# Kernel tuning notes

Measured on AMD Instinct MI355X. Metric: run time of the kernel, lower is better.

Reference implementation:

```python
import jax, jax.numpy as jnp
import numpy as np

N, E, D_IN, H = 4096, 1024, 256, 64
THETA = 0.01
LN_EPS = 1e-5


def _layer_norm(x, w, b):
    m = x.mean(-1, keepdims=True)
    v = ((x - m) ** 2).mean(-1, keepdims=True)
    return (x - m) * jax.lax.rsqrt(v + LN_EPS) * w + b


def setup_inputs() -> dict:
    key = jax.random.key(0)
    ks = jax.random.split(key, 8)
    xav = lambda k, shp: jax.random.normal(k, shp, jnp.float32) * np.float32(np.sqrt(2.0 / (shp[0] + shp[1])))
    return {
        "adj": jax.random.uniform(ks[0], (N, E), jnp.float32),
        "G": jax.random.normal(ks[1], (N, N), jnp.float32) * 0.02,
        "feats": jax.random.normal(ks[2], (N, D_IN), jnp.float32),
        "W_v_w": xav(ks[3], (H, D_IN)),
        "lin_w": xav(ks[4], (H, D_IN)),
        "w_o_w": xav(ks[5], (1, H)),
        "w_o_b": jnp.zeros((1,), jnp.float32),
        "ln1_w": jnp.ones((H,), jnp.float32),
        "ln1_b": jnp.zeros((H,), jnp.float32),
        "ln2_w": jnp.ones((H,), jnp.float32),
        "ln2_b": jnp.zeros((H,), jnp.float32),
        "kn": 10,
    }


def reference(adj, G, feats, W_v_w, lin_w, w_o_w, w_o_b, ln1_w, ln1_b, ln2_w, ln2_b, kn):
    # adj: (N, E) incidence; torch code transposes then uses adj.t() again,
    # so e_center = feats.T @ adj / edge_degree  -> (D_IN, E)
    e_center = (feats.T @ adj) / adj.sum(0)[None, :]
    f = feats @ W_v_w.T                                   # (N, H) values
    scores = (f @ f.T) / np.float32(np.sqrt(H))           # (N, N)
    attn = jax.nn.softmax(scores, axis=1)
    s = _layer_norm(e_center.T @ lin_w.T, ln1_w, ln1_b)   # (E, H)
    d = _layer_norm(attn @ f, ln2_w, ln2_b)               # (N, H)
    # hadamard_power: scores[m,n] = sum_k w[k]*(s[m,k]-d[n,k])^2 + b
    # expanded to avoid the (E*N, H) broadcast the torch code materializes
    w = w_o_w[0]                                          # (H,)
    ta = ((s * s) @ w)[:, None] + ((d * d) @ w)[None, :] - 2.0 * ((s * w) @ d.T) + w_o_b[0]
    ta = jnp.exp(-ta / np.float32(2 * 20 ** 2))           # (E, N)
    Hm = ta.T                                             # (N, E) soft incidence
    # Generate_G_from_H with unit edge weights, done via row/col scaling
    DV = Hm.sum(1)
    DE = Hm.sum(0)
    invDE = jnp.where(DE > 0, 1.0 / DE, 0.0)
    invDV = jnp.where(DV > 0, DV ** -0.5, 0.0)
    A = (invDV[:, None] * Hm) * invDE[None, :]            # DV2 @ H @ W @ invDE
    B = Hm * invDV[:, None]                               # (DV2 @ H).T side
    G_new = A @ B.T                                       # (N, N)
    return (1.0 - THETA) * G + THETA * G_new
```

## Files before the change

kernel.cpp:

```cpp
#include <hip/hip_runtime.h>
#include <hip/hip_bf16.h>
#include <math.h>

#define NN 4096
#define NE 1024
#define DIN 256
#define HD 64

typedef __hip_bfloat16 bf16;
__device__ __forceinline__ float b2f(bf16 x){ return __bfloat162float(x); }

typedef __attribute__((ext_vector_type(8))) short s16x8;
typedef __attribute__((ext_vector_type(4))) float f32x4;

__device__ __forceinline__ unsigned short f2b_rne(float x){
  unsigned u; __builtin_memcpy(&u, &x, 4);
  u += 0x7fff + ((u>>16)&1);
  return (unsigned short)(u>>16);
}

#define STAGE128(dstbase, PA, strideA, PB, strideB, k0) do{ \
  _Pragma("unroll") \
  for (int it_ = 0; it_ < 4; ++it_){ \
    int r_  = it_*32 + (t>>3); \
    int ss_ = ((t&7) ^ (r_&7))*8; \
    __builtin_amdgcn_global_load_lds( \
      (const __attribute__((address_space(1))) void*)((PA) + (size_t)r_*(strideA) + (k0) + ss_), \
      (__attribute__((address_space(3))) void*)((dstbase) + it_*4096 + t*16), 16, 0, 0); \
    __builtin_amdgcn_global_load_lds( \
      (const __attribute__((address_space(1))) void*)((PB) + (size_t)r_*(strideB) + (k0) + ss_), \
      (__attribute__((address_space(3))) void*)((dstbase) + 16384 + it_*4096 + t*16), 16, 0, 0); \
  } }while(0)

#define COMPUTE64(base) do{ \
  _Pragma("unroll") \
  for (int kk_ = 0; kk_ < 2; ++kk_){ \
    s16x8 a_[4], b_[4]; \
    _Pragma("unroll") \
    for (int mi_ = 0; mi_ < 4; ++mi_){ \
      int row_ = wr*64 + mi_*16 + (lane & 15); \
      int s_   = kk_*4 + (lane >> 4); \
      a_[mi_] = *(const s16x8*)((base) + row_*128 + ((s_ ^ (row_&7))*16)); \
    } \
    _Pragma("unroll") \
    for (int ni_ = 0; ni_ < 4; ++ni_){ \
      int row_ = wc*64 + ni_*16 + (lane & 15); \
      int s_   = kk_*4 + (lane >> 4); \
      b_[ni_] = *(const s16x8*)((base) + 16384 + row_*128 + ((s_ ^ (row_&7))*16)); \
    } \
    _Pragma("unroll") \
    for (int mi_ = 0; mi_ < 4; ++mi_) \
      _Pragma("unroll") \
      for (int ni_ = 0; ni_ < 4; ++ni_) \
        acc[mi_][ni_] = __builtin_amdgcn_mfma_f32_16x16x32_bf16(a_[mi_], b_[ni_], acc[mi_][ni_], 0, 0, 0); \
  } }while(0)

__global__ void k_t2b(const float* __restrict__ src, unsigned short* __restrict__ dst,
                      float* __restrict__ csum){
  __shared__ float Ls[64][65];
  int R = gridDim.x*64, C = gridDim.y*64;
  int r0 = blockIdx.x*64, c0 = blockIdx.y*64;
  int t = threadIdx.x;
  int lr = t>>2, lc = (t&3)*16;
  #pragma unroll
  for (int s = 0; s < 4; ++s){
    float4 v = *(const float4*)(src + (size_t)(r0+lr)*C + c0 + lc + s*4);
    Ls[lr][lc+s*4+0]=v.x; Ls[lr][lc+s*4+1]=v.y; Ls[lr][lc+s*4+2]=v.z; Ls[lr][lc+s*4+3]=v.w;
  }
  __syncthreads();
  if (csum != nullptr && t < 64){
    float s = 0.f;
    #pragma unroll
    for (int r = 0; r < 64; ++r) s += Ls[r][t];
    atomicAdd(&csum[c0 + t], s);
  }
  int wc = t>>3, wr8 = (t&7)*8;
  #pragma unroll
  for (int p = 0; p < 2; ++p){
    int c = wc + p*32;
    s16x8 o;
    #pragma unroll
    for (int e = 0; e < 8; ++e) o[e] = (short)f2b_rne(Ls[wr8+e][c]);
    *(s16x8*)(dst + (size_t)(c0+c)*R + r0 + wr8) = o;
  }
}

__global__ void __launch_bounds__(256, 2)
k_ect_mfma(const unsigned short* __restrict__ fT, const unsigned short* __restrict__ aT,
           float* __restrict__ ecT){
  __shared__ __align__(16) unsigned char sm[65536];
  const int t = threadIdx.x, lane = t & 63, w = t >> 6;
  const int wr = w >> 1, wc = w & 1;
  const int m0 = blockIdx.x*128, n0 = blockIdx.y*128, kb = blockIdx.z*256;
  const unsigned short* PA = fT + (size_t)m0*NN + kb;
  const unsigned short* PB = aT + (size_t)n0*NN + kb;
  f32x4 acc[4][4] = {};
  STAGE128(sm, PA, NN, PB, NN, 0);
  __syncthreads();
  int cur = 0;
  for (int kt = 0; kt < 4; ++kt){
    if (kt < 3) STAGE128(sm + (cur^1)*32768, PA, NN, PB, NN, (kt+1)*64);
    COMPUTE64(sm + cur*32768);
    __syncthreads();
    cur ^= 1;
  }
  #pragma unroll
  for (int mi = 0; mi < 4; ++mi)
    #pragma unroll
    for (int q = 0; q < 4; ++q){
      int c = m0 + wr*64 + mi*16 + (lane>>4)*4 + q;
      #pragma unroll
      for (int ni = 0; ni < 4; ++ni){
        int e = n0 + wc*64 + ni*16 + (lane & 15);
        atomicAdd(&ecT[(size_t)e*DIN + c], acc[mi][ni][q]);
      }
    }
}

__global__ void k_s(const float* __restrict__ ecT, const float* __restrict__ colsum,
                    const float* __restrict__ lin_w,
                    const float* __restrict__ ln1w, const float* __restrict__ ln1b,
                    const float* __restrict__ wow,
                    float* __restrict__ sw, float* __restrict__ sq_s){
  int e = blockIdx.x, h = threadIdx.x;
  const float* row = ecT + (size_t)e*DIN;
  const float* lw  = lin_w + (size_t)h*DIN;
  float acc = 0.f;
  for (int c = 0; c < DIN; ++c) acc += row[c]*lw[c];
  acc /= colsum[e];
  float tot = acc;
  for (int m=32;m>=1;m>>=1) tot += __shfl_xor(tot,m);
  float mean = tot*(1.f/64.f);
  float dv = acc - mean;
  float vv = dv*dv;
  for (int m=32;m>=1;m>>=1) vv += __shfl_xor(vv,m);
  float y = dv*(1.f/sqrtf(vv*(1.f/64.f)+1e-5f))*ln1w[h] + ln1b[h];
  float wv = wow[h];
  sw[(size_t)e*HD + h] = y*wv;
  float q = wv*y*y;
  for (int m=32;m>=1;m>>=1) q += __shfl_xor(q,m);
  if (h==0) sq_s[e] = q;
}

__global__ void k_f(const float* __restrict__ feats, const float* __restrict__ Wv,
                    float* __restrict__ f){
  __shared__ float As[64][65];
  __shared__ float Bs[64][65];
  int i0 = blockIdx.x*64;
  int c0 = blockIdx.y*64;
  int tid=threadIdx.x, tx=tid&15, ty=tid>>4;
  float acc[4][4]={};
  for (int idx=tid; idx<4096; idx+=256){
    int r=idx>>6, c=idx&63;
    As[c][r] = feats[(size_t)(i0+r)*DIN + c0+c];
    Bs[c][r] = Wv   [(size_t)r*DIN      + c0+c];
  }
  __syncthreads();
  for (int k=0;k<64;++k){
    float a[4], b[4];
    #pragma unroll
    for (int i=0;i<4;++i) a[i] = As[k][tx*4+i];
    #pragma unroll
    for (int i=0;i<4;++i) b[i] = Bs[k][ty*4+i];
    #pragma unroll
    for (int mi=0;mi<4;++mi)
      #pragma unroll
      for (int ni=0;ni<4;++ni) acc[mi][ni] += a[mi]*b[ni];
  }
  for (int mi=0;mi<4;++mi)
    for (int ni=0;ni<4;++ni)
      atomicAdd(&f[(size_t)(i0+tx*4+mi)*HD + ty*4+ni], acc[mi][ni]);
}

__global__ void k_f2b(const float* __restrict__ f, unsigned short* __restrict__ fb,
                      unsigned short* __restrict__ fbT){
  __shared__ unsigned short Ls[64][72];
  int n0 = blockIdx.x*64;
  int t = threadIdx.x;
  int r = t>>2, c0 = (t&3)*16;
  unsigned short tmp[16];
  #pragma unroll
  for (int s=0;s<16;++s) tmp[s] = f2b_rne(f[(size_t)(n0+r)*HD + c0 + s]);
  s16x8 v0, v1;
  #pragma unroll
  for (int e=0;e<8;++e){ v0[e] = (short)tmp[e]; v1[e] = (short)tmp[8+e]; }
  *(s16x8*)(fb + (size_t)(n0+r)*HD + c0)     = v0;
  *(s16x8*)(fb + (size_t)(n0+r)*HD + c0 + 8) = v1;
  #pragma unroll
  for (int s=0;s<16;++s) Ls[c0+s][r] = tmp[s];
  __syncthreads();
  int h = t>>2, n1 = (t&3)*16;
  s16x8 w0, w1;
  #pragma unroll
  for (int e=0;e<8;++e){ w0[e] = (short)Ls[h][n1+e]; w1[e] = (short)Ls[h][n1+8+e]; }
  *(s16x8*)(fbT + (size_t)h*NN + n0 + n1)     = w0;
  *(s16x8*)(fbT + (size_t)h*NN + n0 + n1 + 8) = w1;
}

__global__ void __launch_bounds__(256)
k_attn(const unsigned short* __restrict__ fb, const unsigned short* __restrict__ fbT,
       float* __restrict__ dpre, float* __restrict__ rowsum){
  __shared__ __align__(16) unsigned char sm[32768];
  const int t  = threadIdx.x;
  const int l  = t & 63;
  const int w  = t >> 6;
  const int g  = l >> 4;
  const int i0 = blockIdx.x*64;
  const int jb0 = blockIdx.y*256;

  s16x8 aQ[2];
  {
    const unsigned short* src = fb + (size_t)(i0 + w*16 + (l&15))*HD + g*8;
    aQ[0] = *(const s16x8*)(src);
    aQ[1] = *(const s16x8*)(src + 32);
  }

  f32x4 acco[4];
  #pragma unroll
  for (int nh=0;nh<4;++nh)
    #pragma unroll
    for (int q=0;q<4;++q) acco[nh][q] = 0.f;
  float rsum[4] = {0.f,0.f,0.f,0.f};

  float* Pw = (float*)(sm + 16384 + w*4096);

  for (int jt = 0; jt < 4; ++jt){
    int j0 = jb0 + jt*64;
    __syncthreads();
    #pragma unroll
    for (int p = 0; p < 2; ++p){
      int r  = p*32 + (t>>3);
      int cs = ((t&7) ^ (r&7))*8;
      __builtin_amdgcn_global_load_lds(
        (const __attribute__((address_space(1))) void*)(fb + (size_t)(j0+r)*HD + cs),
        (__attribute__((address_space(3))) void*)(sm + p*4096 + t*16), 16, 0, 0);
      __builtin_amdgcn_global_load_lds(
        (const __attribute__((address_space(1))) void*)(fbT + (size_t)r*NN + j0 + cs),
        (__attribute__((address_space(3))) void*)(sm + 8192 + p*4096 + t*16), 16, 0, 0);
    }
    __syncthreads();

    f32x4 accs[4];
    #pragma unroll
    for (int nj=0;nj<4;++nj)
      #pragma unroll
      for (int q=0;q<4;++q) accs[nj][q] = 0.f;
    #pragma unroll
    for (int kk=0; kk<2; ++kk){
      int s = kk*4 + g;
      #pragma unroll
      for (int nj=0;nj<4;++nj){
        int row = nj*16 + (l&15);
        s16x8 b = *(const s16x8*)(sm + row*128 + ((s ^ (row&7))*16));
        accs[nj] = __builtin_amdgcn_mfma_f32_16x16x32_bf16(aQ[kk], b, accs[nj], 0,0,0);
      }
    }

    #pragma unroll
    for (int q=0;q<4;++q){
      int i  = g*4 + q;
      int sw = (i&7)<<2;
      #pragma unroll
      for (int nj=0;nj<4;++nj){
        float p = __expf(accs[nj][q]*0.125f);
        rsum[q] += p;
        Pw[i*64 + ((nj*16 + (l&15)) ^ sw)] = p;
      }
    }

    #pragma unroll
    for (int kk=0; kk<2; ++kk){
      int i  = l & 15;
      int sw = (i&7)<<2;
      int jb = g*8 + kk*32;
      f32x4 va = *(const f32x4*)(Pw + i*64 + ( jb      ^ sw));
      f32x4 vb = *(const f32x4*)(Pw + i*64 + ((jb + 4) ^ sw));
      s16x8 pa;
      #pragma unroll
      for (int e=0;e<4;++e){
        float fa = va[e], fbv = vb[e];
        pa[e]   = (short)f2b_rne(fa);
        pa[4+e] = (short)f2b_rne(fbv);
      }
      int s = kk*4 + g;
      #pragma unroll
      for (int nh=0;nh<4;++nh){
        int row = nh*16 + (l&15);
        s16x8 bT = *(const s16x8*)(sm + 8192 + row*128 + ((s ^ (row&7))*16));
        acco[nh] = __builtin_amdgcn_mfma_f32_16x16x32_bf16(pa, bT, acco[nh], 0,0,0);
      }
    }
  }

  #pragma unroll
  for (int q=0;q<4;++q){
    float v = rsum[q];
    v += __shfl_xor(v,1); v += __shfl_xor(v,2);
    v += __shfl_xor(v,4); v += __shfl_xor(v,8);
    if ((l&15)==0) atomicAdd(&rowsum[i0 + w*16 + g*4 + q], v);
  }
  #pragma unroll
  for (int nh=0;nh<4;++nh)
    #pragma unroll
    for (int q=0;q<4;++q)
      atomicAdd(&dpre[(size_t)(i0 + w*16 + g*4 + q)*HD + nh*16 + (l&15)], acco[nh][q]);
}

__global__ void k_dln(const float* __restrict__ dpre, const float* __restrict__ rowsum,
                      const float* __restrict__ ln2w, const float* __restrict__ ln2b,
                      const float* __restrict__ wow,
                      float* __restrict__ dmat, float* __restrict__ sq_d){
  int lane = threadIdx.x & 63;
  int n = blockIdx.x*4 + (threadIdx.x>>6);
  float x = dpre[(size_t)n*HD + lane] / rowsum[n];
  float tot = x;
  for (int m=32;m>=1;m>>=1) tot += __shfl_xor(tot,m);
  float mean = tot*(1.f/64.f);
  float dv = x - mean;
  float vv = dv*dv;
  for (int m=32;m>=1;m>>=1) vv += __shfl_xor(vv,m);
  float y = dv*(1.f/sqrtf(vv*(1.f/64.f)+1e-5f))*ln2w[lane] + ln2b[lane];
  dmat[(size_t)n*HD + lane] = y;
  float wv = wow[lane];
  float q = wv*y*y;
  for (int m=32;m>=1;m>>=1) q += __shfl_xor(q,m);
  if (lane==0) sq_d[n] = q;
}

__global__ void k_hm(const float* __restrict__ dmat, const float* __restrict__ sw,
                     const float* __restrict__ sq_d, const float* __restrict__ sq_s,
                     const float* __restrict__ wob, bf16* __restrict__ Hm){
  __shared__ float As[64][65];
  __shared__ float Bs[64][65];
  int n0 = blockIdx.x*64, e0 = blockIdx.y*64;
  int tid=threadIdx.x, tx=tid&15, ty=tid>>4;
  for (int idx=tid; idx<4096; idx+=256){
    int r=idx>>6, c=idx&63;
    As[c][r] = dmat[(size_t)(n0+r)*HD + c];
    Bs[c][r] = sw  [(size_t)(e0+r)*HD + c];
  }
  __syncthreads();
  float acc[4][4]={};
  for (int k=0;k<64;++k){
    float a[4], b[4];
    #pragma unroll
    for (int i=0;i<4;++i) a[i] = As[k][tx*4+i];
    #pragma unroll
    for (int i=0;i<4;++i) b[i] = Bs[k][ty*4+i];
    #pragma unroll
    for (int mi=0;mi<4;++mi)
      #pragma unroll
      for (int ni=0;ni<4;++ni) acc[mi][ni] += a[mi]*b[ni];
  }
  float bias = wob[0];
  for (int mi=0;mi<4;++mi)
    for (int ni=0;ni<4;++ni){
      int nn = n0+tx*4+mi, ee = e0+ty*4+ni;
      float ta = sq_s[ee] + sq_d[nn] - 2.f*acc[mi][ni] + bias;
      float arg = -ta*(1.f/800.f);
      if (!(arg > -88.f)) arg = -88.f;
      if (arg > 60.f)     arg = 60.f;
      Hm[(size_t)nn*NE + ee] = __float2bfloat16(__expf(arg));
    }
}

__global__ void k_dv(const bf16* __restrict__ Hm, float* __restrict__ invDV){
  __shared__ float sm[256];
  int n = blockIdx.x, t = threadIdx.x;
  const bf16* row = Hm + (size_t)n*NE;
  float a = b2f(row[t]) + b2f(row[t+256]) + b2f(row[t+512]) + b2f(row[t+768]);
  sm[t]=a; __syncthreads();
  for (int s=128;s>0;s>>=1){ if(t<s) sm[t]+=sm[t+s]; __syncthreads(); }
  if (t==0){ float v = sm[0]; invDV[n] = (v>0.f) ? 1.f/sqrtf(v) : 0.f; }
}

__global__ void k_de(const bf16* __restrict__ Hm, float* __restrict__ DE){
  int e  = blockIdx.x*256 + threadIdx.x;
  int i0 = blockIdx.y*128;
  float acc=0.f;
  for (int i=0;i<128;++i) acc += b2f(Hm[(size_t)(i0+i)*NE + e]);
  atomicAdd(&DE[e], acc);
}
__global__ void k_invde(float* __restrict__ DE){
  int e = blockIdx.x*256 + threadIdx.x;
  float v = DE[e];
  DE[e] = (v>0.f) ? rsqrtf(v) : 0.f;
}

__global__ void k_scale(bf16* __restrict__ Hm, const float* __restrict__ rde){
  int idx = blockIdx.x*256 + threadIdx.x;
  int row = idx >> 7, c8 = idx & 127;
  size_t base = (size_t)row*NE + c8*8;
  s16x8 v = *(const s16x8*)(Hm + base);
  s16x8 o;
  #pragma unroll
  for (int j = 0; j < 8; ++j){
    unsigned int ww = ((unsigned int)(unsigned short)v[j]) << 16;
    float fv; __builtin_memcpy(&fv, &ww, 4);
    fv *= rde[c8*8 + j];
    o[j] = (short)f2b_rne(fv);
  }
  *(s16x8*)(Hm + base) = o;
}

__global__ void __launch_bounds__(256, 2)
k_final(const bf16* __restrict__ A2, const float* __restrict__ invDV,
        const float* __restrict__ G, float* __restrict__ out){
  __shared__ __align__(16) unsigned char sm[65536];
  const int t    = threadIdx.x;
  const int lane = t & 63;
  const int w    = t >> 6;
  const int wr   = w >> 1, wc = w & 1;

  int idx = blockIdx.x;
  int bi = (int)(32.5f - sqrtf(32.5f*32.5f - 2.f*(float)idx));
  while ((bi+1)*32 - ((bi+1)*bi)/2 <= idx) ++bi;
  while (bi*32 - (bi*(bi-1))/2 > idx) --bi;
  int bj = bi + (idx - (bi*32 - (bi*(bi-1))/2));
  const int i0 = bi*128, j0 = bj*128;

  const bf16* PA = A2 + (size_t)i0*NE;
  const bf16* PB = A2 + (size_t)j0*NE;

  f32x4 acc[4][4] = {};
  STAGE128(sm, PA, NE, PB, NE, 0);
  __syncthreads();
  int cur = 0;
  for (int kt = 0; kt < 16; ++kt){
    if (kt < 15) STAGE128(sm + (cur^1)*32768, PA, NE, PB, NE, (kt+1)*64);
    COMPUTE64(sm + cur*32768);
    __syncthreads();
    cur ^= 1;
  }

  float dvi[4][4], dvj[4];
  #pragma unroll
  for (int mi = 0; mi < 4; ++mi)
    #pragma unroll
    for (int q = 0; q < 4; ++q)
      dvi[mi][q] = invDV[i0 + wr*64 + mi*16 + (lane>>4)*4 + q];
  #pragma unroll
  for (int ni = 0; ni < 4; ++ni)
    dvj[ni] = invDV[j0 + wc*64 + ni*16 + (lane & 15)];

  #pragma unroll
  for (int mi = 0; mi < 4; ++mi)
    #pragma unroll
    for (int q = 0; q < 4; ++q){
      int ii = i0 + wr*64 + mi*16 + (lane>>4)*4 + q;
      #pragma unroll
      for (int ni = 0; ni < 4; ++ni){
        int jj = j0 + wc*64 + ni*16 + (lane & 15);
        size_t o = (size_t)ii*NN + jj;
        out[o] = 0.99f*G[o] + 0.01f*(dvi[mi][q]*dvj[ni]*acc[mi][ni][q]);
      }
    }

  if (bi == bj) return;
  float (*Mir)[64][65] = (float(*)[64][65])sm;
  for (int p = 0; p < 2; ++p){
    if (wr == p){
      #pragma unroll
      for (int mi = 0; mi < 4; ++mi)
        #pragma unroll
        for (int ni = 0; ni < 4; ++ni)
          #pragma unroll
          for (int q = 0; q < 4; ++q)
            Mir[wc][ni*16 + (lane & 15)][mi*16 + (lane>>4)*4 + q] =
              0.01f*(dvi[mi][q]*dvj[ni]*acc[mi][ni][q]);
    }
    __syncthreads();
    #pragma unroll
    for (int b = 0; b < 2; ++b){
      for (int itr = 0; itr < 16; ++itr){
        int idx2 = itr*256 + t;
        int jl = idx2 >> 6, il = idx2 & 63;
        size_t o = (size_t)(j0 + b*64 + jl)*NN + (i0 + p*64 + il);
        out[o] = 0.99f*G[o] + Mir[b][jl][il];
      }
    }
    __syncthreads();
  }
}

extern "C" void kernel_launch(void* const* d_in, const int* in_sizes, int n_in,
                              void* d_out, int out_size, void* d_ws, size_t ws_size,
                              hipStream_t stream){
  const float* adj  = (const float*)d_in[0];
  const float* G    = (const float*)d_in[1];
  const float* feats= (const float*)d_in[2];
  const float* Wv   = (const float*)d_in[3];
  const float* lin  = (const float*)d_in[4];
  const float* wow  = (const float*)d_in[5];
  const float* wob  = (const float*)d_in[6];
  const float* ln1w = (const float*)d_in[7];
  const float* ln1b = (const float*)d_in[8];
  const float* ln2w = (const float*)d_in[9];
  const float* ln2b = (const float*)d_in[10];
  float* out = (float*)d_out;

  float* w = (float*)d_ws;
  float* colsum = w; w += NE;
  float* DE     = w; w += NE;
  float* sq_s   = w; w += NE;
  float* rowsum = w; w += NN;
  float* sq_d   = w; w += NN;
  float* invDV  = w; w += NN;
  float* ecT    = w; w += NE*DIN;
  float* swp    = w; w += NE*HD;
  float* f      = w; w += NN*HD;
  float* dpre   = w; w += NN*HD;
  float* dmat   = w; w += NN*HD;
  unsigned short* fbm    = (unsigned short*)w; w += NN*HD/2;
  unsigned short* fbT    = (unsigned short*)w; w += NN*HD/2;
  unsigned short* featsT = (unsigned short*)w; w += NN*DIN/2;
  bf16*  Hm     = (bf16*)w;
  unsigned short* adjT = (unsigned short*)Hm;

  hipMemsetAsync(colsum, 0, NE*sizeof(float), stream);
  hipMemsetAsync(DE,     0, NE*sizeof(float), stream);
  hipMemsetAsync(rowsum, 0, NN*sizeof(float), stream);
  hipMemsetAsync(ecT,    0, (size_t)NE*DIN*sizeof(float), stream);
  hipMemsetAsync(f,      0, (size_t)NN*HD*sizeof(float), stream);
  hipMemsetAsync(dpre,   0, (size_t)NN*HD*sizeof(float), stream);

  k_t2b     <<<dim3(64,4),   256, 0, stream>>>(feats, featsT, nullptr);
  k_t2b     <<<dim3(64,16),  256, 0, stream>>>(adj, adjT, colsum);
  k_ect_mfma<<<dim3(2,8,16), 256, 0, stream>>>(featsT, adjT, ecT);
  k_s       <<<NE,            64, 0, stream>>>(ecT, colsum, lin, ln1w, ln1b, wow, swp, sq_s);
  k_f       <<<dim3(64,4),   256, 0, stream>>>(feats, Wv, f);
  k_f2b     <<<64,           256, 0, stream>>>(f, fbm, fbT);
  k_attn    <<<dim3(64,16),  256, 0, stream>>>(fbm, fbT, dpre, rowsum);
  k_dln     <<<NN/4,         256, 0, stream>>>(dpre, rowsum, ln2w, ln2b, wow, dmat, sq_d);
  k_hm      <<<dim3(64,16),  256, 0, stream>>>(dmat, swp, sq_d, sq_s, wob, Hm);
  k_dv      <<<NN,           256, 0, stream>>>(Hm, invDV);
  k_de      <<<dim3(4,32),   256, 0, stream>>>(Hm, DE);
  k_invde   <<<4,            256, 0, stream>>>(DE);
  k_scale   <<<2048,         256, 0, stream>>>(Hm, DE);
  k_final   <<<528,          256, 0, stream>>>(Hm, invDV, G, out);
}
```

Baseline: 354.2 us.

## Use bf16 MFMA for Hm distance GEMM and coalesce final output epilogue

The s·w and d matrices are now stored as bf16, and the Hm kernel computes the cross term with 16x16x32 bf16 MFMA instructions. The B tile is loaded into swizzled LDS through global_load_lds, replacing the fp32 scalar-FMA shared-memory GEMM. Separately, k_final stages the whole 128x128 result tile in LDS and writes both the direct and mirrored output blocks with float4-coalesced reads of G and writes of out. Previously the direct writes were strided scalars and the mirror used two scalar passes. The bf16 cross term adds rounding error to the exponent argument of Hm, and the larger LDS tile may affect occupancy of k_final.

After: 341.6 us. 1.04x faster.

```diff
diff --git a/kernel.cpp b/kernel.cpp
--- a/kernel.cpp
+++ b/kernel.cpp
@@ -121,7 +121,7 @@
                     const float* __restrict__ lin_w,
                     const float* __restrict__ ln1w, const float* __restrict__ ln1b,
                     const float* __restrict__ wow,
-                    float* __restrict__ sw, float* __restrict__ sq_s){
+                    unsigned short* __restrict__ swb, float* __restrict__ sq_s){
   int e = blockIdx.x, h = threadIdx.x;
   const float* row = ecT + (size_t)e*DIN;
   const float* lw  = lin_w + (size_t)h*DIN;
@@ -136,7 +136,7 @@
   for (int m=32;m>=1;m>>=1) vv += __shfl_xor(vv,m);
   float y = dv*(1.f/sqrtf(vv*(1.f/64.f)+1e-5f))*ln1w[h] + ln1b[h];
   float wv = wow[h];
-  sw[(size_t)e*HD + h] = y*wv;
+  swb[(size_t)e*HD + h] = f2b_rne(y*wv);
   float q = wv*y*y;
   for (int m=32;m>=1;m>>=1) q += __shfl_xor(q,m);
   if (h==0) sq_s[e] = q;
@@ -309,7 +309,7 @@
 __global__ void k_dln(const float* __restrict__ dpre, const float* __restrict__ rowsum,
                       const float* __restrict__ ln2w, const float* __restrict__ ln2b,
                       const float* __restrict__ wow,
-                      float* __restrict__ dmat, float* __restrict__ sq_d){
+                      unsigned short* __restrict__ dmatb, float* __restrict__ sq_d){
   int lane = threadIdx.x & 63;
   int n = blockIdx.x*4 + (threadIdx.x>>6);
   float x = dpre[(size_t)n*HD + lane] / rowsum[n];
@@ -320,48 +320,68 @@
   float vv = dv*dv;
   for (int m=32;m>=1;m>>=1) vv += __shfl_xor(vv,m);
   float y = dv*(1.f/sqrtf(vv*(1.f/64.f)+1e-5f))*ln2w[lane] + ln2b[lane];
-  dmat[(size_t)n*HD + lane] = y;
+  dmatb[(size_t)n*HD + lane] = f2b_rne(y);
   float wv = wow[lane];
   float q = wv*y*y;
   for (int m=32;m>=1;m>>=1) q += __shfl_xor(q,m);
   if (lane==0) sq_d[n] = q;
 }
 
-__global__ void k_hm(const float* __restrict__ dmat, const float* __restrict__ sw,
-                     const float* __restrict__ sq_d, const float* __restrict__ sq_s,
-                     const float* __restrict__ wob, bf16* __restrict__ Hm){
-  __shared__ float As[64][65];
-  __shared__ float Bs[64][65];
-  int n0 = blockIdx.x*64, e0 = blockIdx.y*64;
-  int tid=threadIdx.x, tx=tid&15, ty=tid>>4;
-  for (int idx=tid; idx<4096; idx+=256){
-    int r=idx>>6, c=idx&63;
-    As[c][r] = dmat[(size_t)(n0+r)*HD + c];
-    Bs[c][r] = sw  [(size_t)(e0+r)*HD + c];
-  }
-  __syncthreads();
-  float acc[4][4]={};
-  for (int k=0;k<64;++k){
-    float a[4], b[4];
-    #pragma unroll
-    for (int i=0;i<4;++i) a[i] = As[k][tx*4+i];
-    #pragma unroll
-    for (int i=0;i<4;++i) b[i] = Bs[k][ty*4+i];
-    #pragma unroll
-    for (int mi=0;mi<4;++mi)
-      #pragma unroll
-      for (int ni=0;ni<4;++ni) acc[mi][ni] += a[mi]*b[ni];
+__global__ void __launch_bounds__(256)
+k_hm(const unsigned short* __restrict__ dmatb, const unsigned short* __restrict__ swb,
+     const float* __restrict__ sq_d, const float* __restrict__ sq_s,
+     const float* __restrict__ wob, bf16* __restrict__ Hm){
+  __shared__ __align__(16) unsigned char sm[8192];
+  const int t = threadIdx.x, l = t & 63, w = t >> 6, g = l >> 4;
+  const int n0 = blockIdx.x*64, e0 = blockIdx.y*64;
+  #pragma unroll
+  for (int p = 0; p < 2; ++p){
+    int r  = p*32 + (t>>3);
+    int cs = ((t&7) ^ (r&7))*8;
+    __builtin_amdgcn_global_load_lds(
+      (const __attribute__((address_space(1))) void*)(swb + (size_t)(e0+r)*HD + cs),
+      (__attribute__((address_space(3))) void*)(sm + p*4096 + t*16), 16, 0, 0);
+  }
+  s16x8 aQ[2];
+  {
+    const unsigned short* src = dmatb + (size_t)(n0 + w*16 + (l&15))*HD + g*8;
+    aQ[0] = *(const s16x8*)(src);
+    aQ[1] = *(const s16x8*)(src + 32);
+  }
+  f32x4 accs[4];
+  #pragma unroll
+  for (int nj=0;nj<4;++nj)
+    #pragma unroll
+    for (int q=0;q<4;++q) accs[nj][q] = 0.f;
+  __syncthreads();
+  #pragma unroll
+  for (int kk=0; kk<2; ++kk){
+    int s = kk*4 + g;
+    #pragma unroll
+    for (int nj=0;nj<4;++nj){
+      int row = nj*16 + (l&15);
+      s16x8 b = *(const s16x8*)(sm + row*128 + ((s ^ (row&7))*16));
+      accs[nj] = __builtin_amdgcn_mfma_f32_16x16x32_bf16(aQ[kk], b, accs[nj], 0,0,0);
+    }
   }
   float bias = wob[0];
-  for (int mi=0;mi<4;++mi)
-    for (int ni=0;ni<4;++ni){
-      int nn = n0+tx*4+mi, ee = e0+ty*4+ni;
-      float ta = sq_s[ee] + sq_d[nn] - 2.f*acc[mi][ni] + bias;
+  float sqd[4];
+  #pragma unroll
+  for (int q=0;q<4;++q) sqd[q] = sq_d[n0 + w*16 + g*4 + q];
+  #pragma unroll
+  for (int nj=0;nj<4;++nj){
+    int e = e0 + nj*16 + (l&15);
+    float sqs = sq_s[e];
+    #pragma unroll
+    for (int q=0;q<4;++q){
+      float ta = sqs + sqd[q] - 2.f*accs[nj][q] + bias;
       float arg = -ta*(1.f/800.f);
       if (!(arg > -88.f)) arg = -88.f;
       if (arg > 60.f)     arg = 60.f;
-      Hm[(size_t)nn*NE + ee] = __float2bfloat16(__expf(arg));
-    }
+      int n = n0 + w*16 + g*4 + q;
+      Hm[(size_t)n*NE + e] = __float2bfloat16(__expf(arg));
+    }
+  }
 }
 
 __global__ void k_dv(const bf16* __restrict__ Hm, float* __restrict__ invDV){
@@ -406,7 +426,7 @@
 __global__ void __launch_bounds__(256, 2)
 k_final(const bf16* __restrict__ A2, const float* __restrict__ invDV,
         const float* __restrict__ G, float* __restrict__ out){
-  __shared__ __align__(16) unsigned char sm[65536];
+  __shared__ __align__(16) unsigned char sm[128*132*4];
   const int t    = threadIdx.x;
   const int lane = t & 63;
   const int w    = t >> 6;
@@ -443,43 +463,46 @@
   for (int ni = 0; ni < 4; ++ni)
     dvj[ni] = invDV[j0 + wc*64 + ni*16 + (lane & 15)];
 
+  float (*T)[132] = (float(*)[132])sm;
   #pragma unroll
   for (int mi = 0; mi < 4; ++mi)
     #pragma unroll
-    for (int q = 0; q < 4; ++q){
-      int ii = i0 + wr*64 + mi*16 + (lane>>4)*4 + q;
-      #pragma unroll
-      for (int ni = 0; ni < 4; ++ni){
-        int jj = j0 + wc*64 + ni*16 + (lane & 15);
-        size_t o = (size_t)ii*NN + jj;
-        out[o] = 0.99f*G[o] + 0.01f*(dvi[mi][q]*dvj[ni]*acc[mi][ni][q]);
-      }
-    }
+    for (int ni = 0; ni < 4; ++ni)
+      #pragma unroll
+      for (int q = 0; q < 4; ++q)
+        T[wr*64 + mi*16 + (lane>>4)*4 + q][wc*64 + ni*16 + (lane & 15)] =
+          0.01f*(dvi[mi][q]*dvj[ni]*acc[mi][ni][q]);
+  __syncthreads();
+
+  #pragma unroll
+  for (int it = 0; it < 16; ++it){
+    int idx2 = it*256 + t;
+    int il = idx2 >> 5;
+    int jc = (idx2 & 31)*4;
+    size_t o = (size_t)(i0+il)*NN + j0 + jc;
+    float4 gv = *(const float4*)(G + o);
+    float4 r;
+    r.x = 0.99f*gv.x + T[il][jc+0];
+    r.y = 0.99f*gv.y + T[il][jc+1];
+    r.z = 0.99f*gv.z + T[il][jc+2];
+    r.w = 0.99f*gv.w + T[il][jc+3];
+    *(float4*)(out + o) = r;
+  }
 
   if (bi == bj) return;
-  float (*Mir)[64][65] = (float(*)[64][65])sm;
-  for (int p = 0; p < 2; ++p){
-    if (wr == p){
-      #pragma unroll
-      for (int mi = 0; mi < 4; ++mi)
-        #pragma unroll
-        for (int ni = 0; ni < 4; ++ni)
-          #pragma unroll
-          for (int q = 0; q < 4; ++q)
-            Mir[wc][ni*16 + (lane & 15)][mi*16 + (lane>>4)*4 + q] =
-              0.01f*(dvi[mi][q]*dvj[ni]*acc[mi][ni][q]);
-    }
-    __syncthreads();
-    #pragma unroll
-    for (int b = 0; b < 2; ++b){
-      for (int itr = 0; itr < 16; ++itr){
-        int idx2 = itr*256 + t;
-        int jl = idx2 >> 6, il = idx2 & 63;
-        size_t o = (size_t)(j0 + b*64 + jl)*NN + (i0 + p*64 + il);
-        out[o] = 0.99f*G[o] + Mir[b][jl][il];
-      }
-    }
-    __syncthreads();
+  #pragma unroll
+  for (int it = 0; it < 16; ++it){
+    int idx2 = it*256 + t;
+    int jl = idx2 >> 5;
+    int ic = (idx2 & 31)*4;
+    size_t o = (size_t)(j0+jl)*NN + i0 + ic;
+    float4 gv = *(const float4*)(G + o);
+    float4 r;
+    r.x = 0.99f*gv.x + T[ic+0][jl];
+    r.y = 0.99f*gv.y + T[ic+1][jl];
+    r.z = 0.99f*gv.z + T[ic+2][jl];
+    r.w = 0.99f*gv.w + T[ic+3][jl];
+    *(float4*)(out + o) = r;
   }
 }
 
@@ -507,10 +530,10 @@
   float* sq_d   = w; w += NN;
   float* invDV  = w; w += NN;
   float* ecT    = w; w += NE*DIN;
-  float* swp    = w; w += NE*HD;
   float* f      = w; w += NN*HD;
   float* dpre   = w; w += NN*HD;
-  float* dmat   = w; w += NN*HD;
+  unsigned short* swb    = (unsigned short*)w; w += NE*HD/2;
+  unsigned short* dmatb  = (unsigned short*)w; w += NN*HD/2;
   unsigned short* fbm    = (unsigned short*)w; w += NN*HD/2;
   unsigned short* fbT    = (unsigned short*)w; w += NN*HD/2;
   unsigned short* featsT = (unsigned short*)w; w += NN*DIN/2;
@@ -527,12 +550,12 @@
   k_t2b     <<<dim3(64,4),   256, 0, stream>>>(feats, featsT, nullptr);
   k_t2b     <<<dim3(64,16),  256, 0, stream>>>(adj, adjT, colsum);
   k_ect_mfma<<<dim3(2,8,16), 256, 0, stream>>>(featsT, adjT, ecT);
-  k_s       <<<NE,            64, 0, stream>>>(ecT, colsum, lin, ln1w, ln1b, wow, swp, sq_s);
+  k_s       <<<NE,            64, 0, stream>>>(ecT, colsum, lin, ln1w, ln1b, wow, swb, sq_s);
   k_f       <<<dim3(64,4),   256, 0, stream>>>(feats, Wv, f);
   k_f2b     <<<64,           256, 0, stream>>>(f, fbm, fbT);
   k_attn    <<<dim3(64,16),  256, 0, stream>>>(fbm, fbT, dpre, rowsum);
-  k_dln     <<<NN/4,         256, 0, stream>>>(dpre, rowsum, ln2w, ln2b, wow, dmat, sq_d);
-  k_hm      <<<dim3(64,16),  256, 0, stream>>>(dmat, swp, sq_d, sq_s, wob, Hm);
+  k_dln     <<<NN/4,         256, 0, stream>>>(dpre, rowsum, ln2w, ln2b, wow, dmatb, sq_d);
+  k_hm      <<<dim3(64,16),  256, 0, stream>>>(dmatb, swb, sq_d, sq_s, wob, Hm);
   k_dv      <<<NN,           256, 0, stream>>>(Hm, invDV);
   k_de      <<<dim3(4,32),   256, 0, stream>>>(Hm, DE);
   k_invde   <<<4,            256, 0, stream>>>(DE);
```
